# Optimization experiments

Hardware: AMD Instinct MI355X
Metric: run time of the kernel (lower is better)

The kernel has to match this reference:

```python
import jax, jax.numpy as jnp
import numpy as np

N_PAPER = 50000
N_AUTHOR = 50000
E = 400000
N_FEAT = 256
N_HID = 256
N_CLASS = 128
TEMP = 1.0  # cfg.temparature


def setup_inputs() -> dict:
    key = jax.random.key(0)
    ks = jax.random.split(key, 40)
    def lin_init(k, shape, fan_in):
        s = 1.0 / np.sqrt(fan_in)
        return jax.random.uniform(k, shape, jnp.float32, -s, s)
    inp = {}
    inp['x_paper'] = jax.random.normal(ks[0], (N_PAPER, N_FEAT), jnp.float32)
    # xavier-uniform embedding for featureless node type 'author'
    xs = np.sqrt(6.0 / (N_AUTHOR + N_FEAT))
    inp['emb_author'] = jax.random.uniform(ks[1], (N_AUTHOR, N_FEAT), jnp.float32, -xs, xs)
    i = 2
    for l, fin in [(0, N_FEAT), (1, N_HID)]:
        for nt in ['paper', 'author']:
            inp[f'l{l}_root_{nt}_W'] = lin_init(ks[i], (fin, N_HID), fin); i += 1
            inp[f'l{l}_root_{nt}_b'] = lin_init(ks[i], (N_HID,), fin); i += 1
        for et in ['writes', 'rev', 'cites']:
            inp[f'l{l}_rel_{et}_W'] = lin_init(ks[i], (fin, N_HID), fin); i += 1
    inp['out_W'] = lin_init(ks[i], (N_HID, N_CLASS), N_HID); i += 1
    inp['out_b'] = lin_init(ks[i], (N_CLASS,), N_HID); i += 1
    inp['writes_src'] = jax.random.randint(ks[i], (E,), 0, N_AUTHOR); i += 1
    inp['writes_dst'] = jax.random.randint(ks[i], (E,), 0, N_PAPER); i += 1
    inp['rev_src'] = jax.random.randint(ks[i], (E,), 0, N_PAPER); i += 1
    inp['rev_dst'] = jax.random.randint(ks[i], (E,), 0, N_AUTHOR); i += 1
    inp['cites_src'] = jax.random.randint(ks[i], (E,), 0, N_PAPER); i += 1
    inp['cites_dst'] = jax.random.randint(ks[i], (E,), 0, N_PAPER); i += 1
    return inp


def _mean_agg(x_src, src, dst, n_dst):
    # sparse adj_t.matmul(x, reduce='mean'): segment-sum of gathered rows / in-degree (0 for isolated)
    msg = jax.ops.segment_sum(x_src[src], dst, num_segments=n_dst)  # [n_dst, d]
    deg = jax.ops.segment_sum(jnp.ones(src.shape[0], x_src.dtype), dst, num_segments=n_dst)
    return jnp.where(deg[:, None] > 0, msg / jnp.maximum(deg, 1.0)[:, None], 0.0)


def reference(x_paper, emb_author,
              l0_root_paper_W, l0_root_paper_b, l0_root_author_W, l0_root_author_b,
              l0_rel_writes_W, l0_rel_rev_W, l0_rel_cites_W,
              l1_root_paper_W, l1_root_paper_b, l1_root_author_W, l1_root_author_b,
              l1_rel_writes_W, l1_rel_rev_W, l1_rel_cites_W,
              out_W, out_b,
              writes_src, writes_dst, rev_src, rev_dst, cites_src, cites_dst):
    nnodes = {'paper': x_paper.shape[0], 'author': emb_author.shape[0]}
    # (src_type, dst_type, src_idx, dst_idx, rel_slot)
    edges = [('author', 'paper', writes_src, writes_dst, 0),
             ('paper', 'author', rev_src, rev_dst, 1),
             ('paper', 'paper', cites_src, cites_dst, 2)]
    layers = [
        {'root': {'paper': (l0_root_paper_W, l0_root_paper_b), 'author': (l0_root_author_W, l0_root_author_b)},
         'rel': [l0_rel_writes_W, l0_rel_rev_W, l0_rel_cites_W]},
        {'root': {'paper': (l1_root_paper_W, l1_root_paper_b), 'author': (l1_root_author_W, l1_root_author_b)},
         'rel': [l1_rel_writes_W, l1_rel_rev_W, l1_rel_cites_W]},
    ]
    xd = {'paper': x_paper, 'author': emb_author}
    xd_ = dict(xd)  # twin path starts from same features
    hs, hs_ = [], []
    for p in layers:
        out = {k: xd[k] @ p['root'][k][0] + p['root'][k][1] for k in xd}
        out_ = {k: xd_[k] @ p['root'][k][0] + p['root'][k][1] for k in xd_}
        for s, d, src, dst, slot in edges:
            W = p['rel'][slot]
            out[d] = out[d] + _mean_agg(xd[s], src, dst, nnodes[d]) @ W
            out_[d] = out_[d] + xd_[d] @ W  # twin path: no propagation, same rel transform
        xd = {k: jax.nn.relu(v) for k, v in out.items()}   # dropout is identity (eval)
        xd_ = {k: jax.nn.relu(v) for k, v in out_.items()}
        hs.append(xd['paper'])
        hs_.append(xd_['paper'])
    # Summarize: per-node dot-product attention over layer representations
    H = jnp.stack(hs)    # [L, N, d]
    H_ = jnp.stack(hs_)  # [L, N, d]
    alpha = jax.nn.softmax(jnp.sum(H * H_, axis=-1) / TEMP, axis=0)  # [L, N]
    h = jnp.sum(alpha[..., None] * H, axis=0)  # [N, d]
    logits = h @ out_W + out_b
    return (logits, alpha)
```

## Files before the change

### kernel.cpp

```cpp
#include <hip/hip_runtime.h>
#include <hip/hip_bf16.h>

#define NFEAT 256
#define LSTR 72

typedef __attribute__((ext_vector_type(8))) short bf16x8;
typedef __attribute__((ext_vector_type(4))) float f32x4;
typedef __attribute__((ext_vector_type(8))) unsigned short us8;

__device__ __forceinline__ void f2hilo(float x, unsigned short& h, unsigned short& l) {
    __hip_bfloat16 hb = __float2bfloat16(x);
    float hf = __bfloat162float(hb);
    __hip_bfloat16 lb = __float2bfloat16(x - hf);
    h = *reinterpret_cast<unsigned short*>(&hb);
    l = *reinterpret_cast<unsigned short*>(&lb);
}

__global__ __launch_bounds__(256) void cvt8_kernel(
    const float* w0, const float* w1, const float* w2, const float* w3,
    const float* w4, const float* w5, const float* w6, const float* w7,
    unsigned short* base)
{
    int wi = blockIdx.y;
    const float* W = (wi==0)?w0:(wi==1)?w1:(wi==2)?w2:(wi==3)?w3:
                     (wi==4)?w4:(wi==5)?w5:(wi==6)?w6:w7;
    int idx = blockIdx.x * 256 + threadIdx.x;
    int k = idx >> 8, c = idx & 255;
    unsigned short h, l;
    f2hilo(W[idx], h, l);
    unsigned short* Th = base + (size_t)wi * 131072;
    Th[c * 256 + k] = h;
    Th[65536 + c * 256 + k] = l;
}

__global__ __launch_bounds__(256) void cvtfold_kernel(
    const float* a0, const float* a1, const float* a2,
    const float* b0, const float* b1, const float* b2,
    unsigned short* base)
{
    int wi = blockIdx.y;
    int idx = blockIdx.x * 256 + threadIdx.x;
    float v = wi ? (b0[idx] + b1[idx] + b2[idx]) : (a0[idx] + a1[idx] + a2[idx]);
    int k = idx >> 8, c = idx & 255;
    unsigned short h, l;
    f2hilo(v, h, l);
    unsigned short* Th = base + (size_t)(8 + wi) * 131072;
    Th[c * 256 + k] = h;
    Th[65536 + c * 256 + k] = l;
}

__global__ __launch_bounds__(256) void cvtrect_kernel(const float* W, unsigned short* base) {
    int idx = blockIdx.x * 256 + threadIdx.x;
    if (idx >= 256 * 128) return;
    int k = idx >> 7, c = idx & 127;
    unsigned short h, l;
    f2hilo(W[idx], h, l);
    unsigned short* Th = base + (size_t)10 * 131072;
    Th[c * 256 + k] = h;
    Th[65536 + c * 256 + k] = l;
}

__global__ __launch_bounds__(256) void deg_int_kernel(const int* __restrict__ dst,
                                                      int* __restrict__ deg, int nE) {
    int e = blockIdx.x * 256 + threadIdx.x;
    if (e < nE) atomicAdd(&deg[dst[e]], 1);
}

__global__ __launch_bounds__(256) void scan_p1(const int* __restrict__ deg, int n,
                                               int* __restrict__ off, int* __restrict__ bsum) {
    __shared__ int tmp[256];
    int tid = threadIdx.x;
    int i = blockIdx.x * 256 + tid;
    tmp[tid] = (i < n) ? deg[i] : 0;
    __syncthreads();
    #pragma unroll
    for (int ofs = 1; ofs < 256; ofs <<= 1) {
        int t = (tid >= ofs) ? tmp[tid - ofs] : 0;
        __syncthreads();
        tmp[tid] += t;
        __syncthreads();
    }
    if (i < n) off[i + 1] = tmp[tid];
    if (tid == 255) bsum[blockIdx.x] = tmp[255];
}

__global__ __launch_bounds__(256) void scan_p2(int* __restrict__ bA, int nA,
                                               int* __restrict__ bB, int nB,
                                               int* __restrict__ bC, int nC) {
    int* bs; int nb;
    if (blockIdx.x == 0) { bs = bA; nb = nA; }
    else if (blockIdx.x == 1) { bs = bB; nb = nB; }
    else { bs = bC; nb = nC; }
    __shared__ int tmp[256];
    int tid = threadIdx.x;
    tmp[tid] = (tid < nb) ? bs[tid] : 0;
    __syncthreads();
    #pragma unroll
    for (int ofs = 1; ofs < 256; ofs <<= 1) {
        int t = (tid >= ofs) ? tmp[tid - ofs] : 0;
        __syncthreads();
        tmp[tid] += t;
        __syncthreads();
    }
    if (tid < nb) bs[tid] = tmp[tid];
}

__global__ __launch_bounds__(256) void scan_p3(int n, int* __restrict__ off,
                                               const int* __restrict__ bsum) {
    int i = blockIdx.x * 256 + threadIdx.x;
    if (i == 0) off[0] = 0;
    if (i >= n) return;
    int b = blockIdx.x;
    if (b > 0) off[i + 1] += bsum[b - 1];
}

__global__ __launch_bounds__(256) void fill_csr_kernel(const int* __restrict__ src,
                                                       const int* __restrict__ dst, int nE,
                                                       const int* __restrict__ off,
                                                       int* __restrict__ cursor,
                                                       int* __restrict__ list) {
    int e = blockIdx.x * 256 + threadIdx.x;
    if (e >= nE) return;
    int d = dst[e];
    int pos = atomicAdd(&cursor[d], 1);
    list[off[d] + pos] = src[e];
}

__global__ __launch_bounds__(256) void agg_csr_kernel(const float* __restrict__ T,
                                                      const int* __restrict__ off,
                                                      const int* __restrict__ list,
                                                      float* __restrict__ D,
                                                      int mode_add, int do_relu, int M) {
    int r = blockIdx.x * 4 + (threadIdx.x >> 6);
    if (r >= M) return;
    int lane = threadIdx.x & 63;
    int start = off[r], end = off[r + 1];
    float4 acc = make_float4(0.f, 0.f, 0.f, 0.f);
    for (int e = start; e < end; ++e) {
        int s = list[e];
        float4 v = ((const float4*)(T + (size_t)s * NFEAT))[lane];
        acc.x += v.x; acc.y += v.y; acc.z += v.z; acc.w += v.w;
    }
    int cnt = end - start;
    float inv = (cnt > 0) ? 1.0f / (float)cnt : 0.0f;
    float4 d;
    if (mode_add) {
        d = ((float4*)(D + (size_t)r * NFEAT))[lane];
        d.x += acc.x * inv; d.y += acc.y * inv;
        d.z += acc.z * inv; d.w += acc.w * inv;
    } else {
        d.x = acc.x * inv; d.y = acc.y * inv;
        d.z = acc.z * inv; d.w = acc.w * inv;
    }
    if (do_relu) {
        d.x = fmaxf(d.x, 0.f); d.y = fmaxf(d.y, 0.f);
        d.z = fmaxf(d.z, 0.f); d.w = fmaxf(d.w, 0.f);
    }
    ((float4*)(D + (size_t)r * NFEAT))[lane] = d;
}

__global__ __launch_bounds__(256) void alpha_kernel(const float* __restrict__ s0,
                                                    const float* __restrict__ s1,
                                                    float* __restrict__ alpha, int M) {
    int n = blockIdx.x * 256 + threadIdx.x;
    if (n >= M) return;
    float v0 = s0[n], v1 = s1[n];
    float m = fmaxf(v0, v1);
    float e0 = expf(v0 - m), e1 = expf(v1 - m);
    float inv = 1.0f / (e0 + e1);
    alpha[n]     = e0 * inv;
    alpha[M + n] = e1 * inv;
}

struct Seg3 {
    const float *A0, *A1, *A2;
    const unsigned short *Wh0, *Wl0, *Wh1, *Wl1, *Wh2, *Wl2;
};

__global__ __launch_bounds__(256, 2) void gemm_ms(
    Seg3 sp, int nseg, const float* __restrict__ bias, int do_relu,
    float* __restrict__ C, int M, int N)
{
    __shared__ unsigned short Ah[128 * LSTR];
    __shared__ unsigned short Al[128 * LSTR];
    __shared__ unsigned short Bh[128 * LSTR];
    __shared__ unsigned short Bl[128 * LSTR];

    int tid = threadIdx.x;
    int lane = tid & 63;
    int w = tid >> 6;
    int wr = w >> 1, wc = w & 1;
    int row0 = blockIdx.x * 128, col0 = blockIdx.y * 128;
    int fr = lane & 15;
    int fg = lane >> 4;

    int sr = tid & 127;
    int sh = tid >> 7;
    int grow = row0 + sr; if (grow >= M) grow = M - 1;
    int gcol = col0 + sr;

    f32x4 acc[4][4];
    #pragma unroll
    for (int m = 0; m < 4; ++m)
        #pragma unroll
        for (int n = 0; n < 4; ++n)
            acc[m][n] = (f32x4)(0.f);

    for (int s = 0; s < 3; ++s) {
        if (s >= nseg) break;
        const float* Xrow = ((s == 0) ? sp.A0 : (s == 1) ? sp.A1 : sp.A2) + (size_t)grow * NFEAT;
        const unsigned short* WhR = ((s == 0) ? sp.Wh0 : (s == 1) ? sp.Wh1 : sp.Wh2) + (size_t)gcol * NFEAT;
        const unsigned short* WlR = ((s == 0) ? sp.Wl0 : (s == 1) ? sp.Wl1 : sp.Wl2) + (size_t)gcol * NFEAT;

        for (int k0 = 0; k0 < NFEAT; k0 += 32) {
            unsigned short hh[16], ll[16];
            #pragma unroll
            for (int q = 0; q < 4; ++q) {
                float4 v = *(const float4*)(Xrow + k0 + sh * 16 + q * 4);
                f2hilo(v.x, hh[q*4+0], ll[q*4+0]);
                f2hilo(v.y, hh[q*4+1], ll[q*4+1]);
                f2hilo(v.z, hh[q*4+2], ll[q*4+2]);
                f2hilo(v.w, hh[q*4+3], ll[q*4+3]);
            }
            us8 bh0 = *(const us8*)(WhR + k0 + sh * 16);
            us8 bh1 = *(const us8*)(WhR + k0 + sh * 16 + 8);
            us8 bl0 = *(const us8*)(WlR + k0 + sh * 16);
            us8 bl1 = *(const us8*)(WlR + k0 + sh * 16 + 8);
            __syncthreads();
            int wbase = sr * LSTR + sh * 16;
            *(us8*)&Ah[wbase]     = *(us8*)&hh[0];
            *(us8*)&Ah[wbase + 8] = *(us8*)&hh[8];
            *(us8*)&Al[wbase]     = *(us8*)&ll[0];
            *(us8*)&Al[wbase + 8] = *(us8*)&ll[8];
            *(us8*)&Bh[wbase]     = bh0;
            *(us8*)&Bh[wbase + 8] = bh1;
            *(us8*)&Bl[wbase]     = bl0;
            *(us8*)&Bl[wbase + 8] = bl1;
            __syncthreads();

            bf16x8 ahf[4], alf[4], bhf[4], blf[4];
            #pragma unroll
            for (int m = 0; m < 4; ++m) {
                int r = wr * 64 + m * 16 + fr;
                ahf[m] = *(const bf16x8*)&Ah[r * LSTR + fg * 8];
                alf[m] = *(const bf16x8*)&Al[r * LSTR + fg * 8];
            }
            #pragma unroll
            for (int n = 0; n < 4; ++n) {
                int c = wc * 64 + n * 16 + fr;
                bhf[n] = *(const bf16x8*)&Bh[c * LSTR + fg * 8];
                blf[n] = *(const bf16x8*)&Bl[c * LSTR + fg * 8];
            }
            #pragma unroll
            for (int m = 0; m < 4; ++m)
                #pragma unroll
                for (int n = 0; n < 4; ++n) {
                    acc[m][n] = __builtin_amdgcn_mfma_f32_16x16x32_bf16(ahf[m], bhf[n], acc[m][n], 0, 0, 0);
                    acc[m][n] = __builtin_amdgcn_mfma_f32_16x16x32_bf16(alf[m], bhf[n], acc[m][n], 0, 0, 0);
                    acc[m][n] = __builtin_amdgcn_mfma_f32_16x16x32_bf16(ahf[m], blf[n], acc[m][n], 0, 0, 0);
                }
        }
    }

    #pragma unroll
    for (int n = 0; n < 4; ++n) {
        int c = col0 + wc * 64 + n * 16 + fr;
        float bv = bias ? bias[c] : 0.f;
        #pragma unroll
        for (int m = 0; m < 4; ++m) {
            int rbase = row0 + wr * 64 + m * 16 + fg * 4;
            #pragma unroll
            for (int i = 0; i < 4; ++i) {
                int r = rbase + i;
                if (r < M) {
                    float v = acc[m][n][i] + bv;
                    if (do_relu) v = fmaxf(v, 0.f);
                    C[(size_t)r * N + c] = v;
                }
            }
        }
    }
}

__global__ __launch_bounds__(256, 2) void gemm_rowdot_mfma(
    const float* __restrict__ X,
    const unsigned short* __restrict__ Wh, const unsigned short* __restrict__ Wl,
    const float* __restrict__ bias,
    const float* __restrict__ P, const float* __restrict__ Q,
    float* __restrict__ s0g, float* __restrict__ s1g, int M)
{
    __shared__ unsigned short Ah[128 * LSTR];
    __shared__ unsigned short Al[128 * LSTR];
    __shared__ unsigned short Bh[128 * LSTR];
    __shared__ unsigned short Bl[128 * LSTR];
    __shared__ float srow[128];
    __shared__ float s0buf[256];

    int tid = threadIdx.x;
    int lane = tid & 63;
    int w = tid >> 6;
    int wr = w >> 1, wc = w & 1;
    int row0 = blockIdx.x * 128;
    int fr = lane & 15;
    int fg = lane >> 4;

    int sr = tid & 127;
    int sh = tid >> 7;
    int grow = row0 + sr; if (grow >= M) grow = M - 1;

    if (tid < 128) srow[tid] = 0.f;
    float s0part = 0.f;

    const float* Xrow = X + (size_t)grow * NFEAT;
    const float* Qrow = Q + (size_t)grow * NFEAT;

    float rp[4][4];
    #pragma unroll
    for (int m = 0; m < 4; ++m)
        #pragma unroll
        for (int i = 0; i < 4; ++i) rp[m][i] = 0.f;

    for (int ct = 0; ct < 2; ++ct) {
        int col0 = ct * 128;
        const unsigned short* WhR = Wh + (size_t)(col0 + sr) * NFEAT;
        const unsigned short* WlR = Wl + (size_t)(col0 + sr) * NFEAT;

        f32x4 acc[4][4];
        #pragma unroll
        for (int m = 0; m < 4; ++m)
            #pragma unroll
            for (int n = 0; n < 4; ++n)
                acc[m][n] = (f32x4)(0.f);

        for (int k0 = 0; k0 < NFEAT; k0 += 32) {
            unsigned short hh[16], ll[16];
            #pragma unroll
            for (int q = 0; q < 4; ++q) {
                float4 v = *(const float4*)(Xrow + k0 + sh * 16 + q * 4);
                if (ct == 0) {
                    float4 qv = *(const float4*)(Qrow + k0 + sh * 16 + q * 4);
                    s0part += v.x * qv.x + v.y * qv.y + v.z * qv.z + v.w * qv.w;
                }
                f2hilo(v.x, hh[q*4+0], ll[q*4+0]);
                f2hilo(v.y, hh[q*4+1], ll[q*4+1]);
                f2hilo(v.z, hh[q*4+2], ll[q*4+2]);
                f2hilo(v.w, hh[q*4+3], ll[q*4+3]);
            }
            us8 bh0 = *(const us8*)(WhR + k0 + sh * 16);
            us8 bh1 = *(const us8*)(WhR + k0 + sh * 16 + 8);
            us8 bl0 = *(const us8*)(WlR + k0 + sh * 16);
            us8 bl1 = *(const us8*)(WlR + k0 + sh * 16 + 8);
            __syncthreads();
            int wbase = sr * LSTR + sh * 16;
            *(us8*)&Ah[wbase]     = *(us8*)&hh[0];
            *(us8*)&Ah[wbase + 8] = *(us8*)&hh[8];
            *(us8*)&Al[wbase]     = *(us8*)&ll[0];
            *(us8*)&Al[wbase + 8] = *(us8*)&ll[8];
            *(us8*)&Bh[wbase]     = bh0;
            *(us8*)&Bh[wbase + 8] = bh1;
            *(us8*)&Bl[wbase]     = bl0;
            *(us8*)&Bl[wbase + 8] = bl1;
            __syncthreads();

            bf16x8 ahf[4], alf[4], bhf[4], blf[4];
            #pragma unroll
            for (int m = 0; m < 4; ++m) {
                int r = wr * 64 + m * 16 + fr;
                ahf[m] = *(const bf16x8*)&Ah[r * LSTR + fg * 8];
                alf[m] = *(const bf16x8*)&Al[r * LSTR + fg * 8];
            }
            #pragma unroll
            for (int n = 0; n < 4; ++n) {
                int c = wc * 64 + n * 16 + fr;
                bhf[n] = *(const bf16x8*)&Bh[c * LSTR + fg * 8];
                blf[n] = *(const bf16x8*)&Bl[c * LSTR + fg * 8];
            }
            #pragma unroll
            for (int m = 0; m < 4; ++m)
                #pragma unroll
                for (int n = 0; n < 4; ++n) {
                    acc[m][n] = __builtin_amdgcn_mfma_f32_16x16x32_bf16(ahf[m], bhf[n], acc[m][n], 0, 0, 0);
                    acc[m][n] = __builtin_amdgcn_mfma_f32_16x16x32_bf16(alf[m], bhf[n], acc[m][n], 0, 0, 0);
                    acc[m][n] = __builtin_amdgcn_mfma_f32_16x16x32_bf16(ahf[m], blf[n], acc[m][n], 0, 0, 0);
                }
        }

        #pragma unroll
        for (int n = 0; n < 4; ++n) {
            int c = col0 + wc * 64 + n * 16 + fr;
            float bv = bias[c];
            #pragma unroll
            for (int m = 0; m < 4; ++m) {
                #pragma unroll
                for (int i = 0; i < 4; ++i) {
                    int r = row0 + wr * 64 + m * 16 + fg * 4 + i;
                    if (r < M) {
                        float v = fmaxf(acc[m][n][i] + bv, 0.f);
                        rp[m][i] += v * P[(size_t)r * NFEAT + c];
                    }
                }
            }
        }
    }

    s0buf[tid] = s0part;

    #pragma unroll
    for (int o = 1; o < 16; o <<= 1) {
        #pragma unroll
        for (int m = 0; m < 4; ++m)
            #pragma unroll
            for (int i = 0; i < 4; ++i)
                rp[m][i] += __shfl_xor(rp[m][i], o);
    }
    if ((lane & 15) == 0) {
        #pragma unroll
        for (int m = 0; m < 4; ++m)
            #pragma unroll
            for (int i = 0; i < 4; ++i)
                atomicAdd(&srow[wr * 64 + m * 16 + fg * 4 + i], rp[m][i]);
    }
    __syncthreads();
    if (tid < 128 && row0 + tid < M) {
        s1g[row0 + tid] = srow[tid];
        s0g[row0 + tid] = s0buf[tid] + s0buf[tid + 128];
    }
}

__global__ __launch_bounds__(256, 2) void gemm_head(
    const float* __restrict__ P1, const float* __restrict__ P2,
    const float* __restrict__ alpha,
    const unsigned short* __restrict__ Wh, const unsigned short* __restrict__ Wl,
    const float* __restrict__ bias,
    float* __restrict__ C, int M, int N)
{
    __shared__ unsigned short Ah[128 * LSTR];
    __shared__ unsigned short Al[128 * LSTR];
    __shared__ unsigned short Bh[128 * LSTR];
    __shared__ unsigned short Bl[128 * LSTR];

    int tid = threadIdx.x;
    int lane = tid & 63;
    int w = tid >> 6;
    int wr = w >> 1, wc = w & 1;
    int row0 = blockIdx.x * 128;
    int fr = lane & 15;
    int fg = lane >> 4;

    int sr = tid & 127;
    int sh = tid >> 7;
    int grow = row0 + sr; if (grow >= M) grow = M - 1;

    const float* P1row = P1 + (size_t)grow * NFEAT;
    const float* P2row = P2 + (size_t)grow * NFEAT;
    float a0 = alpha[grow], a1 = alpha[M + grow];
    const unsigned short* WhR = Wh + (size_t)sr * NFEAT;
    const unsigned short* WlR = Wl + (size_t)sr * NFEAT;

    f32x4 acc[4][4];
    #pragma unroll
    for (int m = 0; m < 4; ++m)
        #pragma unroll
        for (int n = 0; n < 4; ++n)
            acc[m][n] = (f32x4)(0.f);

    for (int k0 = 0; k0 < NFEAT; k0 += 32) {
        unsigned short hh[16], ll[16];
        #pragma unroll
        for (int q = 0; q < 4; ++q) {
            float4 u = *(const float4*)(P1row + k0 + sh * 16 + q * 4);
            float4 v = *(const float4*)(P2row + k0 + sh * 16 + q * 4);
            float4 x = make_float4(a0*u.x + a1*v.x, a0*u.y + a1*v.y,
                                   a0*u.z + a1*v.z, a0*u.w + a1*v.w);
            f2hilo(x.x, hh[q*4+0], ll[q*4+0]);
            f2hilo(x.y, hh[q*4+1], ll[q*4+1]);
            f2hilo(x.z, hh[q*4+2], ll[q*4+2]);
            f2hilo(x.w, hh[q*4+3], ll[q*4+3]);
        }
        us8 bh0 = *(const us8*)(WhR + k0 + sh * 16);
        us8 bh1 = *(const us8*)(WhR + k0 + sh * 16 + 8);
        us8 bl0 = *(const us8*)(WlR + k0 + sh * 16);
        us8 bl1 = *(const us8*)(WlR + k0 + sh * 16 + 8);
        __syncthreads();
        int wbase = sr * LSTR + sh * 16;
        *(us8*)&Ah[wbase]     = *(us8*)&hh[0];
        *(us8*)&Ah[wbase + 8] = *(us8*)&hh[8];
        *(us8*)&Al[wbase]     = *(us8*)&ll[0];
        *(us8*)&Al[wbase + 8] = *(us8*)&ll[8];
        *(us8*)&Bh[wbase]     = bh0;
        *(us8*)&Bh[wbase + 8] = bh1;
        *(us8*)&Bl[wbase]     = bl0;
        *(us8*)&Bl[wbase + 8] = bl1;
        __syncthreads();

        bf16x8 ahf[4], alf[4], bhf[4], blf[4];
        #pragma unroll
        for (int m = 0; m < 4; ++m) {
            int r = wr * 64 + m * 16 + fr;
            ahf[m] = *(const bf16x8*)&Ah[r * LSTR + fg * 8];
            alf[m] = *(const bf16x8*)&Al[r * LSTR + fg * 8];
        }
        #pragma unroll
        for (int n = 0; n < 4; ++n) {
            int c = wc * 64 + n * 16 + fr;
            bhf[n] = *(const bf16x8*)&Bh[c * LSTR + fg * 8];
            blf[n] = *(const bf16x8*)&Bl[c * LSTR + fg * 8];
        }
        #pragma unroll
        for (int m = 0; m < 4; ++m)
            #pragma unroll
            for (int n = 0; n < 4; ++n) {
                acc[m][n] = __builtin_amdgcn_mfma_f32_16x16x32_bf16(ahf[m], bhf[n], acc[m][n], 0, 0, 0);
                acc[m][n] = __builtin_amdgcn_mfma_f32_16x16x32_bf16(alf[m], bhf[n], acc[m][n], 0, 0, 0);
                acc[m][n] = __builtin_amdgcn_mfma_f32_16x16x32_bf16(ahf[m], blf[n], acc[m][n], 0, 0, 0);
            }
    }

    #pragma unroll
    for (int n = 0; n < 4; ++n) {
        int c = wc * 64 + n * 16 + fr;
        if (c >= N) continue;
        float bv = bias[c];
        #pragma unroll
        for (int m = 0; m < 4; ++m) {
            int rbase = row0 + wr * 64 + m * 16 + fg * 4;
            #pragma unroll
            for (int i = 0; i < 4; ++i) {
                int r = rbase + i;
                if (r < M) C[(size_t)r * N + c] = acc[m][n][i] + bv;
            }
        }
    }
}

extern "C" void kernel_launch(void* const* d_in, const int* in_sizes, int n_in,
                              void* d_out, int out_size, void* d_ws, size_t ws_size,
                              hipStream_t stream)
{
    const float* x_paper    = (const float*)d_in[0];
    const float* emb_author = (const float*)d_in[1];
    const float* W0rp = (const float*)d_in[2];
    const float* b0rp = (const float*)d_in[3];
    const float* W0ra = (const float*)d_in[4];
    const float* b0ra = (const float*)d_in[5];
    const float* W0w  = (const float*)d_in[6];
    const float* W0rev= (const float*)d_in[7];
    const float* W0c  = (const float*)d_in[8];
    const float* W1rp = (const float*)d_in[9];
    const float* b1rp = (const float*)d_in[10];
    const float* W1w  = (const float*)d_in[13];
    const float* W1c  = (const float*)d_in[15];
    const float* outW = (const float*)d_in[16];
    const float* outb = (const float*)d_in[17];
    const int* w_src = (const int*)d_in[18];
    const int* w_dst = (const int*)d_in[19];
    const int* r_src = (const int*)d_in[20];
    const int* r_dst = (const int*)d_in[21];
    const int* c_src = (const int*)d_in[22];
    const int* c_dst = (const int*)d_in[23];

    const int NP = in_sizes[0] / NFEAT;
    const int NA = in_sizes[1] / NFEAT;
    const int NC = in_sizes[17];
    const int nEw = in_sizes[18], nEr = in_sizes[20], nEc = in_sizes[22];

    size_t NB = (size_t)(NP > NA ? NP : NA) * NFEAT;
    float* Z0 = (float*)d_ws;
    float* Z1 = Z0 + NB;
    float* Z2 = Z1 + NB;
    float* s0 = Z2 + NB;
    float* s1 = s0 + NP;
    unsigned short* Wt = (unsigned short*)(s1 + NP);
    #define WT_HI(i) (Wt + (size_t)(i) * 131072)
    #define WT_LO(i) (Wt + (size_t)(i) * 131072 + 65536)
    int* degW = (int*)(Wt + 11 * 131072);
    int* degR = degW + NP;
    int* degC = degR + NA;
    int* curW = degC + NP;
    int* curR = curW + NP;
    int* curC = curR + NA;
    int* offW = curC + NP;
    int* offR = offW + NP + 1;
    int* offC = offR + NA + 1;
    int* bsW  = offC + NP + 1;
    int* bsR  = bsW + 256;
    int* bsC  = bsR + 256;
    int* listW = bsC + 256;
    int* listR = listW + nEw;
    int* listC = listR + nEr;

    float* out   = (float*)d_out;
    float* alpha = out + (size_t)NP * NC;

    hipMemsetAsync(degW, 0, (size_t)2 * (NP + NA + NP) * sizeof(int), stream);
    deg_int_kernel<<<(nEw + 255) / 256, 256, 0, stream>>>(w_dst, degW, nEw);
    deg_int_kernel<<<(nEr + 255) / 256, 256, 0, stream>>>(r_dst, degR, nEr);
    deg_int_kernel<<<(nEc + 255) / 256, 256, 0, stream>>>(c_dst, degC, nEc);

    int nbP = (NP + 255) / 256, nbA = (NA + 255) / 256;
    scan_p1<<<nbP, 256, 0, stream>>>(degW, NP, offW, bsW);
    scan_p1<<<nbA, 256, 0, stream>>>(degR, NA, offR, bsR);
    scan_p1<<<nbP, 256, 0, stream>>>(degC, NP, offC, bsC);
    scan_p2<<<3, 256, 0, stream>>>(bsW, nbP, bsR, nbA, bsC, nbP);
    scan_p3<<<nbP, 256, 0, stream>>>(NP, offW, bsW);
    scan_p3<<<nbA, 256, 0, stream>>>(NA, offR, bsR);
    scan_p3<<<nbP, 256, 0, stream>>>(NP, offC, bsC);

    fill_csr_kernel<<<(nEw + 255) / 256, 256, 0, stream>>>(w_src, w_dst, nEw, offW, curW, listW);
    fill_csr_kernel<<<(nEr + 255) / 256, 256, 0, stream>>>(r_src, r_dst, nEr, offR, curR, listR);
    fill_csr_kernel<<<(nEc + 255) / 256, 256, 0, stream>>>(c_src, c_dst, nEc, offC, curC, listC);

    cvt8_kernel<<<dim3(256, 8), 256, 0, stream>>>(W0rp, W0w, W0c, W0ra, W0rev, W1rp, W1w, W1c, Wt);
    cvtfold_kernel<<<dim3(256, 2), 256, 0, stream>>>(W0rp, W0w, W0c, W1rp, W1w, W1c, Wt);
    cvtrect_kernel<<<128, 256, 0, stream>>>(outW, Wt);

    dim3 blk(256);
    dim3 gP((NP + 127) / 128, 2);
    dim3 gA((NA + 127) / 128, 2);
    dim3 g1((NP + 127) / 128);
    int nodeP = (NP + 3) / 4, nodeA = (NA + 3) / 4;

    agg_csr_kernel<<<nodeP, blk, 0, stream>>>(emb_author, offW, listW, Z0, 0, 0, NP);
    agg_csr_kernel<<<nodeP, blk, 0, stream>>>(x_paper,    offC, listC, Z1, 0, 0, NP);
    {
        Seg3 sp = {x_paper, Z0, Z1, WT_HI(0), WT_LO(0), WT_HI(1), WT_LO(1), WT_HI(2), WT_LO(2)};
        gemm_ms<<<gP, blk, 0, stream>>>(sp, 3, b0rp, 1, Z2, NP, NFEAT);
    }
    agg_csr_kernel<<<nodeA, blk, 0, stream>>>(x_paper, offR, listR, Z0, 0, 0, NA);
    {
        Seg3 sp = {emb_author, Z0, nullptr, WT_HI(3), WT_LO(3), WT_HI(4), WT_LO(4), nullptr, nullptr};
        gemm_ms<<<gA, blk, 0, stream>>>(sp, 2, b0ra, 1, Z1, NA, NFEAT);
    }

    agg_csr_kernel<<<nodeP, blk, 0, stream>>>(Z1, offW, listW, Z0, 0, 0, NP);
    {
        Seg3 sp = {Z2, Z0, nullptr, WT_HI(5), WT_LO(5), WT_HI(6), WT_LO(6), nullptr, nullptr};
        gemm_ms<<<gP, blk, 0, stream>>>(sp, 2, b1rp, 0, Z1, NP, NFEAT);
    }
    {
        Seg3 sp = {Z2, nullptr, nullptr, WT_HI(7), WT_LO(7), nullptr, nullptr, nullptr, nullptr};
        gemm_ms<<<gP, blk, 0, stream>>>(sp, 1, nullptr, 0, Z0, NP, NFEAT);
    }
    agg_csr_kernel<<<nodeP, blk, 0, stream>>>(Z0, offC, listC, Z1, 1, 1, NP);

    {
        Seg3 sp = {x_paper, nullptr, nullptr, WT_HI(8), WT_LO(8), nullptr, nullptr, nullptr, nullptr};
        gemm_ms<<<gP, blk, 0, stream>>>(sp, 1, b0rp, 1, Z0, NP, NFEAT);
    }
    gemm_rowdot_mfma<<<g1, blk, 0, stream>>>(Z0, WT_HI(9), WT_LO(9), b1rp, Z1, Z2, s0, s1, NP);

    alpha_kernel<<<(NP + 255) / 256, blk, 0, stream>>>(s0, s1, alpha, NP);
    gemm_head<<<g1, blk, 0, stream>>>(Z2, Z1, alpha, WT_HI(10), WT_LO(10), outb, out, NP, NC);
}
```

Measured before the change: 1.045 ms.

## Pre-tile weights into MFMA fragment layout and read B directly from global

The weight conversion kernels now write the hi/lo bf16 weights in a tiled layout of 128 columns by 32 k, so each MFMA B fragment can be loaded straight from global memory (through the L2/L1 caches) rather than staged through LDS. The A tile is also stored in LDS in fragment order without padding. Together these shrink shared memory from four padded tiles to two compact ones, and launch bounds rise to 3 blocks per CU for more occupancy. The cost is that B loads now come from global memory inside the inner loop after the barrier, which may add latency, and the unpadded LDS layout may cause bank conflicts.

New measurement: 948.1 us. 1.1x faster.

```diff
diff --git a/kernel.cpp b/kernel.cpp
--- a/kernel.cpp
+++ b/kernel.cpp
@@ -2,7 +2,6 @@
 #include <hip/hip_bf16.h>
 
 #define NFEAT 256
-#define LSTR 72
 
 typedef __attribute__((ext_vector_type(8))) short bf16x8;
 typedef __attribute__((ext_vector_type(4))) float f32x4;
@@ -28,9 +27,10 @@
     int k = idx >> 8, c = idx & 255;
     unsigned short h, l;
     f2hilo(W[idx], h, l);
+    size_t dst = ((size_t)((c >> 7) * 8 + (k >> 5)) * 128 + (c & 127)) * 32 + (k & 31);
     unsigned short* Th = base + (size_t)wi * 131072;
-    Th[c * 256 + k] = h;
-    Th[65536 + c * 256 + k] = l;
+    Th[dst] = h;
+    Th[65536 + dst] = l;
 }
 
 __global__ __launch_bounds__(256) void cvtfold_kernel(
@@ -44,9 +44,10 @@
     int k = idx >> 8, c = idx & 255;
     unsigned short h, l;
     f2hilo(v, h, l);
+    size_t dst = ((size_t)((c >> 7) * 8 + (k >> 5)) * 128 + (c & 127)) * 32 + (k & 31);
     unsigned short* Th = base + (size_t)(8 + wi) * 131072;
-    Th[c * 256 + k] = h;
-    Th[65536 + c * 256 + k] = l;
+    Th[dst] = h;
+    Th[65536 + dst] = l;
 }
 
 __global__ __launch_bounds__(256) void cvtrect_kernel(const float* W, unsigned short* base) {
@@ -55,9 +56,10 @@
     int k = idx >> 7, c = idx & 127;
     unsigned short h, l;
     f2hilo(W[idx], h, l);
+    size_t dst = ((size_t)(k >> 5) * 128 + c) * 32 + (k & 31);
     unsigned short* Th = base + (size_t)10 * 131072;
-    Th[c * 256 + k] = h;
-    Th[65536 + c * 256 + k] = l;
+    Th[dst] = h;
+    Th[65536 + dst] = l;
 }
 
 __global__ __launch_bounds__(256) void deg_int_kernel(const int* __restrict__ dst,
@@ -172,32 +174,31 @@
     alpha[M + n] = e1 * inv;
 }
 
+
 struct Seg3 {
     const float *A0, *A1, *A2;
     const unsigned short *Wh0, *Wl0, *Wh1, *Wl1, *Wh2, *Wl2;
 };
 
-__global__ __launch_bounds__(256, 2) void gemm_ms(
+__global__ __launch_bounds__(256, 3) void gemm_ms(
     Seg3 sp, int nseg, const float* __restrict__ bias, int do_relu,
     float* __restrict__ C, int M, int N)
 {
-    __shared__ unsigned short Ah[128 * LSTR];
-    __shared__ unsigned short Al[128 * LSTR];
-    __shared__ unsigned short Bh[128 * LSTR];
-    __shared__ unsigned short Bl[128 * LSTR];
+    __shared__ unsigned short Ah[128 * 32];
+    __shared__ unsigned short Al[128 * 32];
 
     int tid = threadIdx.x;
     int lane = tid & 63;
     int w = tid >> 6;
     int wr = w >> 1, wc = w & 1;
-    int row0 = blockIdx.x * 128, col0 = blockIdx.y * 128;
+    int row0 = blockIdx.x * 128, cb = blockIdx.y, col0 = cb * 128;
     int fr = lane & 15;
     int fg = lane >> 4;
 
     int sr = tid & 127;
     int sh = tid >> 7;
     int grow = row0 + sr; if (grow >= M) grow = M - 1;
-    int gcol = col0 + sr;
+    int wbase = (((sr >> 4) * 64) + (sh * 2) * 16 + (sr & 15)) * 8;
 
     f32x4 acc[4][4];
     #pragma unroll
@@ -209,8 +210,8 @@
     for (int s = 0; s < 3; ++s) {
         if (s >= nseg) break;
         const float* Xrow = ((s == 0) ? sp.A0 : (s == 1) ? sp.A1 : sp.A2) + (size_t)grow * NFEAT;
-        const unsigned short* WhR = ((s == 0) ? sp.Wh0 : (s == 1) ? sp.Wh1 : sp.Wh2) + (size_t)gcol * NFEAT;
-        const unsigned short* WlR = ((s == 0) ? sp.Wl0 : (s == 1) ? sp.Wl1 : sp.Wl2) + (size_t)gcol * NFEAT;
+        const unsigned short* Wh = (s == 0) ? sp.Wh0 : (s == 1) ? sp.Wh1 : sp.Wh2;
+        const unsigned short* Wl = (s == 0) ? sp.Wl0 : (s == 1) ? sp.Wl1 : sp.Wl2;
 
         for (int k0 = 0; k0 < NFEAT; k0 += 32) {
             unsigned short hh[16], ll[16];
@@ -222,34 +223,28 @@
                 f2hilo(v.z, hh[q*4+2], ll[q*4+2]);
                 f2hilo(v.w, hh[q*4+3], ll[q*4+3]);
             }
-            us8 bh0 = *(const us8*)(WhR + k0 + sh * 16);
-            us8 bh1 = *(const us8*)(WhR + k0 + sh * 16 + 8);
-            us8 bl0 = *(const us8*)(WlR + k0 + sh * 16);
-            us8 bl1 = *(const us8*)(WlR + k0 + sh * 16 + 8);
             __syncthreads();
-            int wbase = sr * LSTR + sh * 16;
-            *(us8*)&Ah[wbase]     = *(us8*)&hh[0];
-            *(us8*)&Ah[wbase + 8] = *(us8*)&hh[8];
-            *(us8*)&Al[wbase]     = *(us8*)&ll[0];
-            *(us8*)&Al[wbase + 8] = *(us8*)&ll[8];
-            *(us8*)&Bh[wbase]     = bh0;
-            *(us8*)&Bh[wbase + 8] = bh1;
-            *(us8*)&Bl[wbase]     = bl0;
-            *(us8*)&Bl[wbase + 8] = bl1;
+            *(us8*)&Ah[wbase]       = *(us8*)&hh[0];
+            *(us8*)&Ah[wbase + 128] = *(us8*)&hh[8];
+            *(us8*)&Al[wbase]       = *(us8*)&ll[0];
+            *(us8*)&Al[wbase + 128] = *(us8*)&ll[8];
             __syncthreads();
 
+            const unsigned short* WhB = Wh + (size_t)(cb * 8 + (k0 >> 5)) * 4096;
+            const unsigned short* WlB = Wl + (size_t)(cb * 8 + (k0 >> 5)) * 4096;
+
             bf16x8 ahf[4], alf[4], bhf[4], blf[4];
             #pragma unroll
             for (int m = 0; m < 4; ++m) {
-                int r = wr * 64 + m * 16 + fr;
-                ahf[m] = *(const bf16x8*)&Ah[r * LSTR + fg * 8];
-                alf[m] = *(const bf16x8*)&Al[r * LSTR + fg * 8];
+                int g = ((wr * 4 + m) * 64 + lane) * 8;
+                ahf[m] = *(const bf16x8*)&Ah[g];
+                alf[m] = *(const bf16x8*)&Al[g];
             }
             #pragma unroll
             for (int n = 0; n < 4; ++n) {
-                int c = wc * 64 + n * 16 + fr;
-                bhf[n] = *(const bf16x8*)&Bh[c * LSTR + fg * 8];
-                blf[n] = *(const bf16x8*)&Bl[c * LSTR + fg * 8];
+                int o = (wc * 64 + n * 16 + fr) * 32 + fg * 8;
+                bhf[n] = *(const bf16x8*)(WhB + o);
+                blf[n] = *(const bf16x8*)(WlB + o);
             }
             #pragma unroll
             for (int m = 0; m < 4; ++m)
@@ -282,17 +277,15 @@
     }
 }
 
-__global__ __launch_bounds__(256, 2) void gemm_rowdot_mfma(
+__global__ __launch_bounds__(256, 3) void gemm_rowdot_mfma(
     const float* __restrict__ X,
     const unsigned short* __restrict__ Wh, const unsigned short* __restrict__ Wl,
     const float* __restrict__ bias,
     const float* __restrict__ P, const float* __restrict__ Q,
     float* __restrict__ s0g, float* __restrict__ s1g, int M)
 {
-    __shared__ unsigned short Ah[128 * LSTR];
-    __shared__ unsigned short Al[128 * LSTR];
-    __shared__ unsigned short Bh[128 * LSTR];
-    __shared__ unsigned short Bl[128 * LSTR];
+    __shared__ unsigned short Ah[128 * 32];
+    __shared__ unsigned short Al[128 * 32];
     __shared__ float srow[128];
     __shared__ float s0buf[256];
 
@@ -307,6 +300,7 @@
     int sr = tid & 127;
     int sh = tid >> 7;
     int grow = row0 + sr; if (grow >= M) grow = M - 1;
+    int wbase = (((sr >> 4) * 64) + (sh * 2) * 16 + (sr & 15)) * 8;
 
     if (tid < 128) srow[tid] = 0.f;
     float s0part = 0.f;
@@ -321,10 +315,6 @@
         for (int i = 0; i < 4; ++i) rp[m][i] = 0.f;
 
     for (int ct = 0; ct < 2; ++ct) {
-        int col0 = ct * 128;
-        const unsigned short* WhR = Wh + (size_t)(col0 + sr) * NFEAT;
-        const unsigned short* WlR = Wl + (size_t)(col0 + sr) * NFEAT;
-
         f32x4 acc[4][4];
         #pragma unroll
         for (int m = 0; m < 4; ++m)
@@ -346,34 +336,28 @@
                 f2hilo(v.z, hh[q*4+2], ll[q*4+2]);
                 f2hilo(v.w, hh[q*4+3], ll[q*4+3]);
             }
-            us8 bh0 = *(const us8*)(WhR + k0 + sh * 16);
-            us8 bh1 = *(const us8*)(WhR + k0 + sh * 16 + 8);
-            us8 bl0 = *(const us8*)(WlR + k0 + sh * 16);
-            us8 bl1 = *(const us8*)(WlR + k0 + sh * 16 + 8);
             __syncthreads();
-            int wbase = sr * LSTR + sh * 16;
-            *(us8*)&Ah[wbase]     = *(us8*)&hh[0];
-            *(us8*)&Ah[wbase + 8] = *(us8*)&hh[8];
-            *(us8*)&Al[wbase]     = *(us8*)&ll[0];
-            *(us8*)&Al[wbase + 8] = *(us8*)&ll[8];
-            *(us8*)&Bh[wbase]     = bh0;
-            *(us8*)&Bh[wbase + 8] = bh1;
-            *(us8*)&Bl[wbase]     = bl0;
-            *(us8*)&Bl[wbase + 8] = bl1;
+            *(us8*)&Ah[wbase]       = *(us8*)&hh[0];
+            *(us8*)&Ah[wbase + 128] = *(us8*)&hh[8];
+            *(us8*)&Al[wbase]       = *(us8*)&ll[0];
+            *(us8*)&Al[wbase + 128] = *(us8*)&ll[8];
             __syncthreads();
 
+            const unsigned short* WhB = Wh + (size_t)(ct * 8 + (k0 >> 5)) * 4096;
+            const unsigned short* WlB = Wl + (size_t)(ct * 8 + (k0 >> 5)) * 4096;
+
             bf16x8 ahf[4], alf[4], bhf[4], blf[4];
             #pragma unroll
             for (int m = 0; m < 4; ++m) {
-                int r = wr * 64 + m * 16 + fr;
-                ahf[m] = *(const bf16x8*)&Ah[r * LSTR + fg * 8];
-                alf[m] = *(const bf16x8*)&Al[r * LSTR + fg * 8];
+                int g = ((wr * 4 + m) * 64 + lane) * 8;
+                ahf[m] = *(const bf16x8*)&Ah[g];
+                alf[m] = *(const bf16x8*)&Al[g];
             }
             #pragma unroll
             for (int n = 0; n < 4; ++n) {
-                int c = wc * 64 + n * 16 + fr;
-                bhf[n] = *(const bf16x8*)&Bh[c * LSTR + fg * 8];
-                blf[n] = *(const bf16x8*)&Bl[c * LSTR + fg * 8];
+                int o = (wc * 64 + n * 16 + fr) * 32 + fg * 8;
+                bhf[n] = *(const bf16x8*)(WhB + o);
+                blf[n] = *(const bf16x8*)(WlB + o);
             }
             #pragma unroll
             for (int m = 0; m < 4; ++m)
@@ -385,6 +369,7 @@
                 }
         }
 
+        int col0 = ct * 128;
         #pragma unroll
         for (int n = 0; n < 4; ++n) {
             int c = col0 + wc * 64 + n * 16 + fr;
@@ -427,17 +412,15 @@
     }
 }
 
-__global__ __launch_bounds__(256, 2) void gemm_head(
+__global__ __launch_bounds__(256, 3) void gemm_head(
     const float* __restrict__ P1, const float* __restrict__ P2,
     const float* __restrict__ alpha,
     const unsigned short* __restrict__ Wh, const unsigned short* __restrict__ Wl,
     const float* __restrict__ bias,
     float* __restrict__ C, int M, int N)
 {
-    __shared__ unsigned short Ah[128 * LSTR];
-    __shared__ unsigned short Al[128 * LSTR];
-    __shared__ unsigned short Bh[128 * LSTR];
-    __shared__ unsigned short Bl[128 * LSTR];
+    __shared__ unsigned short Ah[128 * 32];
+    __shared__ unsigned short Al[128 * 32];
 
     int tid = threadIdx.x;
     int lane = tid & 63;
@@ -450,12 +433,11 @@
     int sr = tid & 127;
     int sh = tid >> 7;
     int grow = row0 + sr; if (grow >= M) grow = M - 1;
+    int wbase = (((sr >> 4) * 64) + (sh * 2) * 16 + (sr & 15)) * 8;
 
     const float* P1row = P1 + (size_t)grow * NFEAT;
     const float* P2row = P2 + (size_t)grow * NFEAT;
     float a0 = alpha[grow], a1 = alpha[M + grow];
-    const unsigned short* WhR = Wh + (size_t)sr * NFEAT;
-    const unsigned short* WlR = Wl + (size_t)sr * NFEAT;
 
     f32x4 acc[4][4];
     #pragma unroll
@@ -477,34 +459,28 @@
             f2hilo(x.z, hh[q*4+2], ll[q*4+2]);
             f2hilo(x.w, hh[q*4+3], ll[q*4+3]);
         }
-        us8 bh0 = *(const us8*)(WhR + k0 + sh * 16);
-        us8 bh1 = *(const us8*)(WhR + k0 + sh * 16 + 8);
-        us8 bl0 = *(const us8*)(WlR + k0 + sh * 16);
-        us8 bl1 = *(const us8*)(WlR + k0 + sh * 16 + 8);
         __syncthreads();
-        int wbase = sr * LSTR + sh * 16;
-        *(us8*)&Ah[wbase]     = *(us8*)&hh[0];
-        *(us8*)&Ah[wbase + 8] = *(us8*)&hh[8];
-        *(us8*)&Al[wbase]     = *(us8*)&ll[0];
-        *(us8*)&Al[wbase + 8] = *(us8*)&ll[8];
-        *(us8*)&Bh[wbase]     = bh0;
-        *(us8*)&Bh[wbase + 8] = bh1;
-        *(us8*)&Bl[wbase]     = bl0;
-        *(us8*)&Bl[wbase + 8] = bl1;
+        *(us8*)&Ah[wbase]       = *(us8*)&hh[0];
+        *(us8*)&Ah[wbase + 128] = *(us8*)&hh[8];
+        *(us8*)&Al[wbase]       = *(us8*)&ll[0];
+        *(us8*)&Al[wbase + 128] = *(us8*)&ll[8];
         __syncthreads();
 
+        const unsigned short* WhB = Wh + (size_t)(k0 >> 5) * 4096;
+        const unsigned short* WlB = Wl + (size_t)(k0 >> 5) * 4096;
+
         bf16x8 ahf[4], alf[4], bhf[4], blf[4];
         #pragma unroll
         for (int m = 0; m < 4; ++m) {
-            int r = wr * 64 + m * 16 + fr;
-            ahf[m] = *(const bf16x8*)&Ah[r * LSTR + fg * 8];
-            alf[m] = *(const bf16x8*)&Al[r * LSTR + fg * 8];
+            int g = ((wr * 4 + m) * 64 + lane) * 8;
+            ahf[m] = *(const bf16x8*)&Ah[g];
+            alf[m] = *(const bf16x8*)&Al[g];
         }
         #pragma unroll
         for (int n = 0; n < 4; ++n) {
-            int c = wc * 64 + n * 16 + fr;
-            bhf[n] = *(const bf16x8*)&Bh[c * LSTR + fg * 8];
-            blf[n] = *(const bf16x8*)&Bl[c * LSTR + fg * 8];
+            int o = (wc * 64 + n * 16 + fr) * 32 + fg * 8;
+            bhf[n] = *(const bf16x8*)(WhB + o);
+            blf[n] = *(const bf16x8*)(WlB + o);
         }
         #pragma unroll
         for (int m = 0; m < 4; ++m)
```
